# Performance work log

Measured on AMD Instinct MI355X. Metric: run time of the kernel, lower is better.

Reference implementation:

```python
import jax, jax.numpy as jnp
import numpy as np

T, N, I, H = 512, 512, 256, 256


def setup_inputs() -> dict:
    key = jax.random.key(0)
    k_in, k_h, k_d, k_wi, k_wh, k_bi, k_bh = jax.random.split(key, 7)
    inputs = jax.random.normal(k_in, (T * N, I), dtype=jnp.float32)
    hidden_state = jax.random.normal(k_h, (N, H), dtype=jnp.float32)
    done = (jax.random.uniform(k_d, (T * N,)) < 0.005).astype(jnp.float32)
    s = 1.0 / np.sqrt(H)
    W_ih = jax.random.uniform(k_wi, (3 * H, I), minval=-s, maxval=s, dtype=jnp.float32)
    W_hh = jax.random.uniform(k_wh, (3 * H, H), minval=-s, maxval=s, dtype=jnp.float32)
    b_ih = jax.random.uniform(k_bi, (3 * H,), minval=-s, maxval=s, dtype=jnp.float32)
    b_hh = jax.random.uniform(k_bh, (3 * H,), minval=-s, maxval=s, dtype=jnp.float32)
    return {"inputs": inputs, "hidden_state": hidden_state, "done": done,
            "W_ih": W_ih, "W_hh": W_hh, "b_ih": b_ih, "b_hh": b_hh}


def reference(inputs, hidden_state, done, W_ih, W_hh, b_ih, b_hh):
    # inputs: (T*N, I), hidden_state: (N, H), done: (T*N,)
    x = inputs.reshape(T, N, I)
    d = done.reshape(T, N)
    # Precompute input contributions for all steps in one big GEMM: (T, N, 3H)
    gi = jnp.einsum('tni,gi->tng', x, W_ih) + b_ih

    def step(h, td):
        gi_t, d_t = td
        # inline hidden-state reset at episode boundaries (done flag)
        h = h * (1.0 - d_t)[:, None]
        gh = h @ W_hh.T + b_hh  # (N, 3H)
        i_r, i_z, i_n = jnp.split(gi_t, 3, axis=-1)
        h_r, h_z, h_n = jnp.split(gh, 3, axis=-1)
        r = jax.nn.sigmoid(i_r + h_r)
        z = jax.nn.sigmoid(i_z + h_z)
        n = jnp.tanh(i_n + r * h_n)
        h_new = (1.0 - z) * n + z * h
        return h_new, h_new

    h_final, outs = jax.lax.scan(step, hidden_state, (gi, d))
    output = outs.reshape(T * N, H)
    return output, h_final
```

## Files before the change

### kernel.cpp

```cpp
#include <hip/hip_runtime.h>

#define kT 512
#define kN 512
#define kH 256
#define SBL 128
#define SQ 4

typedef float  f32x4  __attribute__((ext_vector_type(4)));
typedef __bf16 bf16x8 __attribute__((ext_vector_type(8)));
typedef __bf16 bf16x4 __attribute__((ext_vector_type(4)));
typedef __bf16 bf16x2 __attribute__((ext_vector_type(2)));

static __device__ __forceinline__ float sigm(float x) {
  float e = __builtin_amdgcn_exp2f(-1.4426950408889634f * x);
  return __builtin_amdgcn_rcpf(1.0f + e);
}
static __device__ __forceinline__ float tanh_fast(float x) {
  float e = __builtin_amdgcn_exp2f(-2.8853900817779268f * x);
  return fmaf(2.0f, __builtin_amdgcn_rcpf(1.0f + e), -1.0f);
}
static __device__ __forceinline__ float sel4(f32x4 v, int k) {
  float a = (k & 1) ? v[1] : v[0];
  float b = (k & 1) ? v[3] : v[2];
  return (k & 2) ? b : a;
}
static __device__ __forceinline__ float sel4b(bf16x4 v, int k) {
  float a = (k & 1) ? (float)v[1] : (float)v[0];
  float b = (k & 1) ? (float)v[3] : (float)v[2];
  return (k & 2) ? b : a;
}

__global__ __launch_bounds__(512) void gi_gemm(
    const float* __restrict__ x, const float* __restrict__ Wih,
    const float* __restrict__ bih, const float* __restrict__ bhh,
    __bf16* __restrict__ gis)
{
  __shared__ __align__(16) __bf16 Al[128][264];
  __shared__ __align__(16) __bf16 Bl[128][264];
  const int tid  = threadIdx.x;
  const int lane = tid & 63, w = tid >> 6;
  const int wm = w & 1, wn = w >> 1;
  const int c = lane & 15, lg = lane >> 4;
  const long R0 = (long)blockIdx.x * 128;
  const int t  = (int)(R0 >> 9);
  const int n0 = (int)(R0 & 511);

  #pragma unroll
  for (int it = 0; it < 16; ++it) {
    int slot = tid + it * 512;
    int r  = slot >> 6;
    int kq = (slot & 63) * 4;
    float4 av = *(const float4*)(x + (R0 + r) * 256 + kq);
    bf16x4 a4 = {(__bf16)av.x, (__bf16)av.y, (__bf16)av.z, (__bf16)av.w};
    *(bf16x4*)(&Al[r][kq]) = a4;
  }

  for (int nb = 0; nb < 6; ++nb) {
    __syncthreads();
    #pragma unroll
    for (int it = 0; it < 16; ++it) {
      int slot = tid + it * 512;
      int r  = slot >> 6;
      int kq = (slot & 63) * 4;
      float4 bv = *(const float4*)(Wih + (long)(nb * 128 + r) * 256 + kq);
      bf16x4 b4 = {(__bf16)bv.x, (__bf16)bv.y, (__bf16)bv.z, (__bf16)bv.w};
      *(bf16x4*)(&Bl[r][kq]) = b4;
    }
    __syncthreads();

    const int gate = nb >> 1;
    f32x4 acc[4][2];
    #pragma unroll
    for (int nt = 0; nt < 2; ++nt) {
      int j = nb * 128 + wn * 32 + nt * 16 + c;
      float bv = bih[j] + (gate < 2 ? bhh[j] : 0.0f);
      #pragma unroll
      for (int mt = 0; mt < 4; ++mt) acc[mt][nt] = (f32x4){bv, bv, bv, bv};
    }

    #pragma unroll
    for (int ss = 0; ss < 8; ++ss) {
      bf16x8 af[4], bfr[2];
      #pragma unroll
      for (int mt = 0; mt < 4; ++mt)
        af[mt] = *(const bf16x8*)(&Al[wm * 64 + mt * 16 + c][ss * 32 + lg * 8]);
      #pragma unroll
      for (int nt = 0; nt < 2; ++nt)
        bfr[nt] = *(const bf16x8*)(&Bl[wn * 32 + nt * 16 + c][ss * 32 + lg * 8]);
      #pragma unroll
      for (int mt = 0; mt < 4; ++mt)
        #pragma unroll
        for (int nt = 0; nt < 2; ++nt)
          acc[mt][nt] = __builtin_amdgcn_mfma_f32_16x16x32_bf16(af[mt], bfr[nt], acc[mt][nt], 0, 0, 0);
    }

    const int w2g = (nb & 1) * 4 + wn;
    #pragma unroll
    for (int mt = 0; mt < 4; ++mt) {
      const int S16 = n0 + wm * 64 + mt * 16;
      const long blk4 = (S16 >> 2) + lg;
      #pragma unroll
      for (int nt = 0; nt < 2; ++nt) {
        bf16x4 v;
        #pragma unroll
        for (int i = 0; i < 4; ++i) v[i] = (__bf16)acc[mt][nt][i];
        long dest = (((long)t * 128 + blk4) * 8 + w2g) * 384 +
                    (gate * 2 + nt) * 64 + c * 4;
        *(bf16x4*)(gis + dest) = v;
      }
    }
  }
}

__global__ __attribute__((amdgpu_waves_per_eu(2, 2))) __launch_bounds__(512)
void gru_scan(
    const __bf16* __restrict__ gis, const float* __restrict__ h0,
    const float* __restrict__ done, const float* __restrict__ Whh,
    const float* __restrict__ bhh, float* __restrict__ out)
{
  __shared__ __align__(16) __bf16 hbuf[2][SQ * 256];
  __shared__ __align__(16) unsigned char h8buf[2][SQ * 256];
  __shared__ __align__(16) unsigned char wr8[8 * 8 * 64 * 16];
  __shared__ unsigned char doneL[kT * SQ];

  const int tid  = threadIdx.x;
  const int lane = tid & 63, w2 = tid >> 6;
  const int b   = blockIdx.x;
  const int nb4 = b * SQ;
  const int c = lane & 15, lg = lane >> 4;
  const int jh0 = w2 * 32 + c, jh1 = jh0 + 16;
  const int sr = c & 3;

  f32x4 wfn[16], wfz[16];
  #pragma unroll
  for (int tp = 0; tp < 2; ++tp) {
    const int jn = 512 + w2 * 32 + tp * 16 + c;
    const int jz = 256 + w2 * 32 + tp * 16 + c;
    const int jr =       w2 * 32 + tp * 16 + c;
    #pragma unroll
    for (int ss = 0; ss < 8; ++ss) {
      const int k0 = ss * 32 + lg * 8;
      float4 n0_ = *(const float4*)(Whh + (long)jn * 256 + k0);
      float4 n1_ = *(const float4*)(Whh + (long)jn * 256 + k0 + 4);
      bf16x8 vn = {(__bf16)n0_.x, (__bf16)n0_.y, (__bf16)n0_.z, (__bf16)n0_.w,
                   (__bf16)n1_.x, (__bf16)n1_.y, (__bf16)n1_.z, (__bf16)n1_.w};
      wfn[tp * 8 + ss] = __builtin_bit_cast(f32x4, vn);
      float4 z0 = *(const float4*)(Whh + (long)jz * 256 + k0);
      float4 z1 = *(const float4*)(Whh + (long)jz * 256 + k0 + 4);
      bf16x8 vz = {(__bf16)z0.x, (__bf16)z0.y, (__bf16)z0.z, (__bf16)z0.w,
                   (__bf16)z1.x, (__bf16)z1.y, (__bf16)z1.z, (__bf16)z1.w};
      wfz[tp * 8 + ss] = __builtin_bit_cast(f32x4, vz);
      float4 r0_ = *(const float4*)(Whh + (long)jr * 256 + k0);
      float4 r1_ = *(const float4*)(Whh + (long)jr * 256 + k0 + 4);
      int rl = __builtin_amdgcn_cvt_pk_fp8_f32(r0_.x, r0_.y, 0, 0);
      rl     = __builtin_amdgcn_cvt_pk_fp8_f32(r0_.z, r0_.w, rl, 1);
      int rh = __builtin_amdgcn_cvt_pk_fp8_f32(r1_.x, r1_.y, 0, 0);
      rh     = __builtin_amdgcn_cvt_pk_fp8_f32(r1_.z, r1_.w, rh, 1);
      int2 rp = {rl, rh};
      *(int2*)(&wr8[(((w2 * 8 + ss) * 64) + lane) * 16 + tp * 8]) = rp;
    }
  }
  #pragma unroll
  for (int i = 0; i < 16; ++i) {
    asm volatile("" : "+a"(wfn[i]));
    asm volatile("" : "+a"(wfz[i]));
  }
  const float bn0 = bhh[512 + jh0];
  const float bn1 = bhh[512 + jh1];

  for (int idx = tid; idx < (kT - 1) * SQ; idx += 512) {
    int tt = idx >> 2, s = idx & 3;
    doneL[idx] = (unsigned char)(done[(long)(tt + 1) * kN + nb4 + s] != 0.0f);
  }
  if (tid < SQ) doneL[(kT - 1) * SQ + tid] = 0;

  {
    const int s  = tid >> 7;
    const int k2 = (tid & 127) * 2;
    float sc = 1.0f - done[nb4 + s];
    const float* hp = h0 + (long)(nb4 + s) * 256 + k2;
    float f0 = hp[0] * sc, f1 = hp[1] * sc;
    bf16x2 v = {(__bf16)f0, (__bf16)f1};
    *(bf16x2*)(&hbuf[0][s * 256 + (((k2 * 2) ^ (s << 4)) >> 1)]) = v;
    int pk = __builtin_amdgcn_cvt_pk_fp8_f32(f0, f1, 0, 0);
    *(unsigned short*)(&h8buf[0][s * 256 + (k2 ^ (s << 3))]) = (unsigned short)(pk & 0xffff);
  }
  float hold0, hold1;
  {
    float sc = 1.0f - done[nb4 + lg];
    hold0 = h0[(long)(nb4 + lg) * 256 + jh0] * sc;
    hold1 = h0[(long)(nb4 + lg) * 256 + jh1] * sc;
  }
  __syncthreads();

  const long cstep = 128L * 8 * 384;
  const __bf16* gcb = gis + ((long)b * 8 + w2) * 384 + c * 4;
  bf16x4 p00 = *(const bf16x4*)(gcb);
  bf16x4 p01 = *(const bf16x4*)(gcb + 64);
  bf16x4 p10 = *(const bf16x4*)(gcb + 128);
  bf16x4 p11 = *(const bf16x4*)(gcb + 192);
  bf16x4 pn0 = *(const bf16x4*)(gcb + 256);
  bf16x4 pn1 = *(const bf16x4*)(gcb + 320);

  const unsigned char* wrb = &wr8[w2 * 8192];

  #pragma unroll 1
  for (int t = 0; t < kT; ++t) {
    bf16x4 q00 = p00, q01 = p01, q10 = p10, q11 = p11, qn0 = pn0, qn1 = pn1;
    unsigned du = *(const unsigned*)(&doneL[t * SQ]);

    {
      const long tn = (t < kT - 1) ? (t + 1) : t;
      const __bf16* gc = gcb + tn * cstep;
      p00 = *(const bf16x4*)(gc);
      p01 = *(const bf16x4*)(gc + 64);
      p10 = *(const bf16x4*)(gc + 128);
      p11 = *(const bf16x4*)(gc + 192);
      pn0 = *(const bf16x4*)(gc + 256);
      pn1 = *(const bf16x4*)(gc + 320);
    }

    f32x4 ar0, ar1, az0, az1, an0, an1;
    #pragma unroll
    for (int i = 0; i < 4; ++i) {
      ar0[i] = (float)q00[i]; ar1[i] = (float)q01[i];
      az0[i] = (float)q10[i]; az1[i] = (float)q11[i];
    }
    an0 = (f32x4){bn0, bn0, bn0, bn0};
    an1 = (f32x4){bn1, bn1, bn1, bn1};
    asm volatile("" : "+v"(ar0), "+v"(ar1), "+v"(az0), "+v"(az1), "+v"(an0), "+v"(an1));

    {
      const __bf16* hb = &hbuf[t & 1][0];
      const unsigned char* h8b = &h8buf[t & 1][0];
      #pragma unroll
      for (int ss = 0; ss < 8; ++ss) {
        int cb = (ss * 64 + lg * 16) ^ (sr << 4);
        bf16x8 afr = *(const bf16x8*)(hb + sr * 256 + (cb >> 1));
        long   a8  = *(const long*)(h8b + sr * 256 + ((ss * 32 + lg * 8) ^ (sr << 3)));
        int4  brp = *(const int4*)(wrb + (ss * 64 + lane) * 16);
        int2  b0i = {brp.x, brp.y};
        int2  b1i = {brp.z, brp.w};
        long  br0 = __builtin_bit_cast(long, b0i);
        long  br1 = __builtin_bit_cast(long, b1i);
        ar0 = __builtin_amdgcn_mfma_f32_16x16x32_fp8_fp8(a8, br0, ar0, 0, 0, 0);
        ar1 = __builtin_amdgcn_mfma_f32_16x16x32_fp8_fp8(a8, br1, ar1, 0, 0, 0);
        az0 = __builtin_amdgcn_mfma_f32_16x16x32_bf16(afr, __builtin_bit_cast(bf16x8, wfz[ss]),     az0, 0, 0, 0);
        az1 = __builtin_amdgcn_mfma_f32_16x16x32_bf16(afr, __builtin_bit_cast(bf16x8, wfz[8 + ss]), az1, 0, 0, 0);
        an0 = __builtin_amdgcn_mfma_f32_16x16x32_bf16(afr, __builtin_bit_cast(bf16x8, wfn[ss]),     an0, 0, 0, 0);
        an1 = __builtin_amdgcn_mfma_f32_16x16x32_bf16(afr, __builtin_bit_cast(bf16x8, wfn[8 + ss]), an1, 0, 0, 0);
      }
    }

    {
      float* op = out + ((long)t * kN + nb4) * kH;
      __bf16* hw = &hbuf[(t & 1) ^ 1][0];
      unsigned char* h8w = &h8buf[(t & 1) ^ 1][0];
      const float dn = (float)((du >> (lg * 8)) & 255u);
      float r0 = sigm(sel4(ar0, lg));
      float r1 = sigm(sel4(ar1, lg));
      float z0 = sigm(sel4(az0, lg));
      float z1 = sigm(sel4(az1, lg));
      float n0v = tanh_fast(sel4b(qn0, lg) + r0 * sel4(an0, lg));
      float n1v = tanh_fast(sel4b(qn1, lg) + r1 * sel4(an1, lg));
      float hn0 = n0v + z0 * (hold0 - n0v);
      float hn1 = n1v + z1 * (hold1 - n1v);
      float hk0 = hn0 * (1.0f - dn);
      float hk1 = hn1 * (1.0f - dn);
      hold0 = hk0;
      hold1 = hk1;
      op[(long)lg * kH + jh0] = hn0;
      op[(long)lg * kH + jh1] = hn1;
      hw[(lg * 512 + ((jh0 * 2) ^ (lg << 4))) >> 1] = (__bf16)hk0;
      hw[(lg * 512 + ((jh1 * 2) ^ (lg << 4))) >> 1] = (__bf16)hk1;
      int pk8 = __builtin_amdgcn_cvt_pk_fp8_f32(hk0, hk1, 0, 0);
      h8w[lg * 256 + (jh0 ^ (lg << 3))] = (unsigned char)(pk8 & 255);
      h8w[lg * 256 + (jh1 ^ (lg << 3))] = (unsigned char)((pk8 >> 8) & 255);
    }

    asm volatile("s_waitcnt lgkmcnt(0)" ::: "memory");
    asm volatile("s_barrier" ::: "memory");
  }

  {
    float* outF = out + (long)kT * kN * kH;
    outF[(long)(nb4 + lg) * kH + jh0] = hold0;
    outF[(long)(nb4 + lg) * kH + jh1] = hold1;
  }
}

__global__ __launch_bounds__(256) void gru_naive(
    const float* __restrict__ x, const float* __restrict__ h0,
    const float* __restrict__ done, const float* __restrict__ Wih,
    const float* __restrict__ Whh, const float* __restrict__ bih,
    const float* __restrict__ bhh, float* __restrict__ out)
{
  __shared__ float hsA[16][257];
  __shared__ float hsB[16][257];
  const int tid = threadIdx.x;
  const int b = blockIdx.x, nb = b * 16;
  for (int s = 0; s < 16; ++s)
    hsA[s][tid] = h0[(long)(nb + s) * 256 + tid] * (1.0f - done[nb + s]);
  __syncthreads();
  float (*hr)[257] = hsA;
  float (*hw)[257] = hsB;
  float* outF = out + (long)kT * kN * kH;
  for (int t = 0; t < kT; ++t) {
    for (int s = 0; s < 16; ++s) {
      const float* xr = x + ((long)t * kN + nb + s) * 256;
      float pr  = bih[tid] + bhh[tid];
      float pz  = bih[256 + tid] + bhh[256 + tid];
      float pnx = bih[512 + tid];
      float pnh = bhh[512 + tid];
      const float* wr = Wih + (long)tid * 256;
      const float* wz = Wih + (long)(256 + tid) * 256;
      const float* wn = Wih + (long)(512 + tid) * 256;
      const float* vr = Whh + (long)tid * 256;
      const float* vz = Whh + (long)(256 + tid) * 256;
      const float* vn = Whh + (long)(512 + tid) * 256;
      #pragma unroll 4
      for (int k = 0; k < 256; ++k) {
        float xv = xr[k], hv = hr[s][k];
        pr  = fmaf(xv, wr[k], pr);  pr  = fmaf(hv, vr[k], pr);
        pz  = fmaf(xv, wz[k], pz);  pz  = fmaf(hv, vz[k], pz);
        pnx = fmaf(xv, wn[k], pnx); pnh = fmaf(hv, vn[k], pnh);
      }
      float r = sigm(pr), z = sigm(pz);
      float n = tanh_fast(pnx + r * pnh);
      float ho = hr[s][tid];
      float hn = n + z * (ho - n);
      out[((long)t * kN + nb + s) * 256 + tid] = hn;
      if (t == kT - 1) outF[(long)(nb + s) * 256 + tid] = hn;
      float d = (t < kT - 1) ? done[(long)(t + 1) * kN + nb + s] : 0.0f;
      hw[s][tid] = hn * (1.0f - d);
    }
    __syncthreads();
    float (*tmp)[257] = hr; hr = hw; hw = tmp;
  }
}

extern "C" void kernel_launch(void* const* d_in, const int* in_sizes, int n_in,
                              void* d_out, int out_size, void* d_ws, size_t ws_size,
                              hipStream_t stream) {
  const float* x    = (const float*)d_in[0];
  const float* h0   = (const float*)d_in[1];
  const float* done = (const float*)d_in[2];
  const float* Wih  = (const float*)d_in[3];
  const float* Whh  = (const float*)d_in[4];
  const float* bih  = (const float*)d_in[5];
  const float* bhh  = (const float*)d_in[6];
  float* out = (float*)d_out;

  const size_t GI_BYTES = (size_t)kT * kN * 768 * 2;
  if (ws_size >= GI_BYTES) {
    __bf16* gis = (__bf16*)d_ws;
    hipLaunchKernelGGL(gi_gemm, dim3(2048), dim3(512), 0, stream, x, Wih, bih, bhh, gis);
    hipLaunchKernelGGL(gru_scan, dim3(SBL), dim3(512), 0, stream, gis, h0, done, Whh, bhh, out);
  } else {
    hipLaunchKernelGGL(gru_naive, dim3(32), dim3(256), 0, stream, x, h0, done, Wih, Whh, bih, bhh, out);
  }
}
```

Baseline: 1.025 ms.

## Halve sequences per scan block to spread the GRU recurrence over more CUs

Each GRU scan block now handles 2 sequences instead of 4, which doubles the grid so more compute units take part. The precomputed gate buffer layout in the input GEMM is changed to match the new 2-sequence blocking. In the recurrent step each thread now does one gate/update element instead of two, which shortens the per-step elementwise tail on the serial critical path. In exchange, half the MFMA tile rows do duplicated work, since the same number of MFMAs now produce only two useful rows. The recurrent weights are also loaded and converted by twice as many blocks.

```diff
diff --git a/kernel.cpp b/kernel.cpp
--- a/kernel.cpp
+++ b/kernel.cpp
@@ -3,8 +3,8 @@
 #define kT 512
 #define kN 512
 #define kH 256
-#define SBL 128
-#define SQ 4
+#define SBL 256
+#define SQ 2
 
 typedef float  f32x4  __attribute__((ext_vector_type(4)));
 typedef __bf16 bf16x8 __attribute__((ext_vector_type(8)));
@@ -19,15 +19,8 @@
   float e = __builtin_amdgcn_exp2f(-2.8853900817779268f * x);
   return fmaf(2.0f, __builtin_amdgcn_rcpf(1.0f + e), -1.0f);
 }
-static __device__ __forceinline__ float sel4(f32x4 v, int k) {
-  float a = (k & 1) ? v[1] : v[0];
-  float b = (k & 1) ? v[3] : v[2];
-  return (k & 2) ? b : a;
-}
-static __device__ __forceinline__ float sel4b(bf16x4 v, int k) {
-  float a = (k & 1) ? (float)v[1] : (float)v[0];
-  float b = (k & 1) ? (float)v[3] : (float)v[2];
-  return (k & 2) ? b : a;
+static __device__ __forceinline__ float sel01(f32x4 v, int s) {
+  return s ? v[1] : v[0];
 }
 
 __global__ __launch_bounds__(512) void gi_gemm(
@@ -98,15 +91,16 @@
     #pragma unroll
     for (int mt = 0; mt < 4; ++mt) {
       const int S16 = n0 + wm * 64 + mt * 16;
-      const long blk4 = (S16 >> 2) + lg;
+      const long blk2 = (S16 >> 1) + lg * 2;
       #pragma unroll
       for (int nt = 0; nt < 2; ++nt) {
-        bf16x4 v;
-        #pragma unroll
-        for (int i = 0; i < 4; ++i) v[i] = (__bf16)acc[mt][nt][i];
-        long dest = (((long)t * 128 + blk4) * 8 + w2g) * 384 +
-                    (gate * 2 + nt) * 64 + c * 4;
-        *(bf16x4*)(gis + dest) = v;
+        bf16x2 v0 = {(__bf16)acc[mt][nt][0], (__bf16)acc[mt][nt][1]};
+        bf16x2 v1 = {(__bf16)acc[mt][nt][2], (__bf16)acc[mt][nt][3]};
+        long base0 = (((long)t * 256 + blk2) * 8 + w2g) * 192 +
+                     (gate * 2 + nt) * 32 + c * 2;
+        long base1 = base0 + 8 * 192;
+        *(bf16x2*)(gis + base0) = v0;
+        *(bf16x2*)(gis + base1) = v1;
       }
     }
   }
@@ -126,10 +120,13 @@
   const int tid  = threadIdx.x;
   const int lane = tid & 63, w2 = tid >> 6;
   const int b   = blockIdx.x;
-  const int nb4 = b * SQ;
+  const int nb2 = b * SQ;
   const int c = lane & 15, lg = lane >> 4;
   const int jh0 = w2 * 32 + c, jh1 = jh0 + 16;
-  const int sr = c & 3;
+  const int sr = c & 1;
+  const int s  = lg & 1;
+  const int ch = lg >> 1;
+  const int jh = w2 * 32 + ch * 16 + c;
 
   f32x4 wfn[16], wfz[16];
   #pragma unroll
@@ -169,62 +166,68 @@
   const float bn1 = bhh[512 + jh1];
 
   for (int idx = tid; idx < (kT - 1) * SQ; idx += 512) {
-    int tt = idx >> 2, s = idx & 3;
-    doneL[idx] = (unsigned char)(done[(long)(tt + 1) * kN + nb4 + s] != 0.0f);
+    int tt = idx >> 1, sq = idx & 1;
+    doneL[idx] = (unsigned char)(done[(long)(tt + 1) * kN + nb2 + sq] != 0.0f);
   }
   if (tid < SQ) doneL[(kT - 1) * SQ + tid] = 0;
 
   {
-    const int s  = tid >> 7;
-    const int k2 = (tid & 127) * 2;
-    float sc = 1.0f - done[nb4 + s];
-    const float* hp = h0 + (long)(nb4 + s) * 256 + k2;
-    float f0 = hp[0] * sc, f1 = hp[1] * sc;
-    bf16x2 v = {(__bf16)f0, (__bf16)f1};
-    *(bf16x2*)(&hbuf[0][s * 256 + (((k2 * 2) ^ (s << 4)) >> 1)]) = v;
-    int pk = __builtin_amdgcn_cvt_pk_fp8_f32(f0, f1, 0, 0);
-    *(unsigned short*)(&h8buf[0][s * 256 + (k2 ^ (s << 3))]) = (unsigned short)(pk & 0xffff);
-  }
-  float hold0, hold1;
+    const int sq = tid >> 8;
+    const int k2 = (tid & 255) * 2;
+    if (k2 < 256) {
+      float sc = 1.0f - done[nb2 + sq];
+      const float* hp = h0 + (long)(nb2 + sq) * 256 + k2;
+      float f0 = hp[0] * sc, f1 = hp[1] * sc;
+      bf16x2 v = {(__bf16)f0, (__bf16)f1};
+      *(bf16x2*)(&hbuf[0][(sq * 512 + ((k2 * 2) ^ (sq << 4))) >> 1]) = v;
+      int pk = __builtin_amdgcn_cvt_pk_fp8_f32(f0, f1, 0, 0);
+      *(unsigned short*)(&h8buf[0][sq * 256 + (k2 ^ (sq << 3))]) = (unsigned short)(pk & 0xffff);
+    }
+  }
+  float hold;
   {
-    float sc = 1.0f - done[nb4 + lg];
-    hold0 = h0[(long)(nb4 + lg) * 256 + jh0] * sc;
-    hold1 = h0[(long)(nb4 + lg) * 256 + jh1] * sc;
+    float sc = 1.0f - done[nb2 + s];
+    hold = h0[(long)(nb2 + s) * 256 + jh] * sc;
   }
   __syncthreads();
 
-  const long cstep = 128L * 8 * 384;
-  const __bf16* gcb = gis + ((long)b * 8 + w2) * 384 + c * 4;
-  bf16x4 p00 = *(const bf16x4*)(gcb);
-  bf16x4 p01 = *(const bf16x4*)(gcb + 64);
-  bf16x4 p10 = *(const bf16x4*)(gcb + 128);
-  bf16x4 p11 = *(const bf16x4*)(gcb + 192);
-  bf16x4 pn0 = *(const bf16x4*)(gcb + 256);
-  bf16x4 pn1 = *(const bf16x4*)(gcb + 320);
+  const long cstep = 256L * 8 * 192;
+  const __bf16* gcb = gis + ((long)b * 8 + w2) * 192 + c * 2;
+  bf16x2 p00 = *(const bf16x2*)(gcb);
+  bf16x2 p01 = *(const bf16x2*)(gcb + 32);
+  bf16x2 p10 = *(const bf16x2*)(gcb + 64);
+  bf16x2 p11 = *(const bf16x2*)(gcb + 96);
+  bf16x2 pn0 = *(const bf16x2*)(gcb + 128);
+  bf16x2 pn1 = *(const bf16x2*)(gcb + 160);
 
   const unsigned char* wrb = &wr8[w2 * 8192];
 
   #pragma unroll 1
   for (int t = 0; t < kT; ++t) {
-    bf16x4 q00 = p00, q01 = p01, q10 = p10, q11 = p11, qn0 = pn0, qn1 = pn1;
-    unsigned du = *(const unsigned*)(&doneL[t * SQ]);
+    bf16x2 q00 = p00, q01 = p01, q10 = p10, q11 = p11, qn0 = pn0, qn1 = pn1;
+    unsigned short du2 = *(const unsigned short*)(&doneL[t * SQ]);
 
     {
       const long tn = (t < kT - 1) ? (t + 1) : t;
       const __bf16* gc = gcb + tn * cstep;
-      p00 = *(const bf16x4*)(gc);
-      p01 = *(const bf16x4*)(gc + 64);
-      p10 = *(const bf16x4*)(gc + 128);
-      p11 = *(const bf16x4*)(gc + 192);
-      pn0 = *(const bf16x4*)(gc + 256);
-      pn1 = *(const bf16x4*)(gc + 320);
+      p00 = *(const bf16x2*)(gc);
+      p01 = *(const bf16x2*)(gc + 32);
+      p10 = *(const bf16x2*)(gc + 64);
+      p11 = *(const bf16x2*)(gc + 96);
+      pn0 = *(const bf16x2*)(gc + 128);
+      pn1 = *(const bf16x2*)(gc + 160);
     }
 
     f32x4 ar0, ar1, az0, az1, an0, an1;
-    #pragma unroll
-    for (int i = 0; i < 4; ++i) {
-      ar0[i] = (float)q00[i]; ar1[i] = (float)q01[i];
-      az0[i] = (float)q10[i]; az1[i] = (float)q11[i];
+    {
+      float r00 = (float)q00[0], r01 = (float)q00[1];
+      float r10 = (float)q01[0], r11 = (float)q01[1];
+      float z00 = (float)q10[0], z01 = (float)q10[1];
+      float z10 = (float)q11[0], z11 = (float)q11[1];
+      ar0 = (f32x4){r00, r01, r00, r01};
+      ar1 = (f32x4){r10, r11, r10, r11};
+      az0 = (f32x4){z00, z01, z00, z01};
+      az1 = (f32x4){z10, z11, z10, z11};
     }
     an0 = (f32x4){bn0, bn0, bn0, bn0};
     an1 = (f32x4){bn1, bn1, bn1, bn1};
@@ -253,29 +256,22 @@
     }
 
     {
-      float* op = out + ((long)t * kN + nb4) * kH;
+      float* op = out + ((long)t * kN + nb2) * kH;
       __bf16* hw = &hbuf[(t & 1) ^ 1][0];
       unsigned char* h8w = &h8buf[(t & 1) ^ 1][0];
-      const float dn = (float)((du >> (lg * 8)) & 255u);
-      float r0 = sigm(sel4(ar0, lg));
-      float r1 = sigm(sel4(ar1, lg));
-      float z0 = sigm(sel4(az0, lg));
-      float z1 = sigm(sel4(az1, lg));
-      float n0v = tanh_fast(sel4b(qn0, lg) + r0 * sel4(an0, lg));
-      float n1v = tanh_fast(sel4b(qn1, lg) + r1 * sel4(an1, lg));
-      float hn0 = n0v + z0 * (hold0 - n0v);
-      float hn1 = n1v + z1 * (hold1 - n1v);
-      float hk0 = hn0 * (1.0f - dn);
-      float hk1 = hn1 * (1.0f - dn);
-      hold0 = hk0;
-      hold1 = hk1;
-      op[(long)lg * kH + jh0] = hn0;
-      op[(long)lg * kH + jh1] = hn1;
-      hw[(lg * 512 + ((jh0 * 2) ^ (lg << 4))) >> 1] = (__bf16)hk0;
-      hw[(lg * 512 + ((jh1 * 2) ^ (lg << 4))) >> 1] = (__bf16)hk1;
-      int pk8 = __builtin_amdgcn_cvt_pk_fp8_f32(hk0, hk1, 0, 0);
-      h8w[lg * 256 + (jh0 ^ (lg << 3))] = (unsigned char)(pk8 & 255);
-      h8w[lg * 256 + (jh1 ^ (lg << 3))] = (unsigned char)((pk8 >> 8) & 255);
+      const float dn = (float)((du2 >> (s * 8)) & 255u);
+      float rv = sigm(ch ? sel01(ar1, s) : sel01(ar0, s));
+      float zv = sigm(ch ? sel01(az1, s) : sel01(az0, s));
+      float gn = ch ? (float)(s ? qn1[1] : qn1[0]) : (float)(s ? qn0[1] : qn0[0]);
+      float hv = ch ? sel01(an1, s) : sel01(an0, s);
+      float nv = tanh_fast(gn + rv * hv);
+      float hn = nv + zv * (hold - nv);
+      float hk = hn * (1.0f - dn);
+      hold = hk;
+      op[(long)s * kH + jh] = hn;
+      hw[(s * 512 + ((jh * 2) ^ (s << 4))) >> 1] = (__bf16)hk;
+      int pk8 = __builtin_amdgcn_cvt_pk_fp8_f32(hk, hk, 0, 0);
+      h8w[s * 256 + (jh ^ (s << 3))] = (unsigned char)(pk8 & 255);
     }
 
     asm volatile("s_waitcnt lgkmcnt(0)" ::: "memory");
@@ -284,8 +280,7 @@
 
   {
     float* outF = out + (long)kT * kN * kH;
-    outF[(long)(nb4 + lg) * kH + jh0] = hold0;
-    outF[(long)(nb4 + lg) * kH + jh1] = hold1;
+    outF[(long)(nb2 + s) * kH + jh] = hold;
   }
 }
 
```

After: 894.2 us. 12.7% less time.
